# Kernel optimization log

Hardware: AMD Instinct MI355X
Metric: run time of the kernel (lower is better)

## Reference

```python
import jax, jax.numpy as jnp
import numpy as np

VOCAB = 50257
FEAT = 512
EPS = 1e-12  # F.normalize default eps


def setup_inputs() -> dict:
    key = jax.random.key(0)
    k1, k2, k3 = jax.random.split(key, 3)
    token_ids = jax.random.randint(k1, (32, 4096), 0, VOCAB)
    # nn.Linear(vocab, feat): weight [FEAT, VOCAB], bias [FEAT]
    W = jax.random.normal(k2, (FEAT, VOCAB), dtype=jnp.float32) * 0.02
    b = jax.random.normal(k3, (FEAT,), dtype=jnp.float32) * 0.02
    return {"token_ids": token_ids, "W": W, "b": b}


def reference(token_ids, W, b):
    # one_hot(ids) @ W.T + b  ==  gather rows of W.T at ids, then add bias
    feats = W.T[token_ids] + b  # [B, S, FEAT]
    norm = jnp.sqrt(jnp.sum(feats * feats, axis=-1, keepdims=True))
    return feats / jnp.maximum(norm, EPS)
```

## Files before the change

### kernel.cpp

```cpp
#include <hip/hip_runtime.h>
#include <hip/hip_bf16.h>

#define VOCAB 50257
#define FEAT 512
#define NTOK (32 * 4096)
#define EPS 1e-12f
#define NFT 8

typedef float f32x4 __attribute__((ext_vector_type(4)));

__device__ __forceinline__ unsigned short f2bf(float x) {
    __hip_bfloat16 h = __float2bfloat16(x);
    unsigned short u; __builtin_memcpy(&u, &h, 2); return u;
}
__device__ __forceinline__ float bfround(float x) {
    return __bfloat162float(__float2bfloat16(x));
}
__device__ __forceinline__ float bflo(unsigned int w) {
    unsigned int u = w << 16; float f; __builtin_memcpy(&f, &u, 4); return f;
}
__device__ __forceinline__ float bfhi(unsigned int w) {
    unsigned int u = w & 0xffff0000u; float f; __builtin_memcpy(&f, &u, 4); return f;
}

__global__ __launch_bounds__(256) void transpose_bias_bf16(
        const float* __restrict__ W, const float* __restrict__ b,
        unsigned short* __restrict__ Wt, float* __restrict__ partial) {
    __shared__ float tile[64][65];
    __shared__ float psum[4][64];
    const int t = threadIdx.x, l = t & 63, w = t >> 6;
    const int v0 = blockIdx.x * 64, f0 = blockIdx.y * 64;
    const int c = l & 15, r = l >> 4;
    const int vb = v0 + c * 4;

    float p[4] = {0.f, 0.f, 0.f, 0.f};
#pragma unroll
    for (int k = 0; k < 4; ++k) {
        const int fl = w * 16 + k * 4 + r;
        const int f  = f0 + fl;
        f32x4 x;
        if (vb + 3 < VOCAB) {
            __builtin_memcpy(&x, W + (size_t)f * VOCAB + vb, 16);
        } else {
#pragma unroll
            for (int q = 0; q < 4; ++q)
                x[q] = (vb + q < VOCAB) ? W[(size_t)f * VOCAB + vb + q] : 0.0f;
        }
        const float bf = b[f];
#pragma unroll
        for (int q = 0; q < 4; ++q) {
            const float xi = x[q] + bf;
            tile[fl][c * 4 + q] = xi;
            const float xr = bfround(xi);
            p[q] += xr * xr;
        }
    }
#pragma unroll
    for (int q = 0; q < 4; ++q) {
        float s = p[q];
        s += __shfl_xor(s, 16, 64);
        s += __shfl_xor(s, 32, 64);
        if (r == 0) psum[w][c * 4 + q] = s;
    }
    __syncthreads();
    if (t < 64) {
        const int v = v0 + t;
        if (v < VOCAB)
            partial[blockIdx.y * VOCAB + v] =
                psum[0][t] + psum[1][t] + psum[2][t] + psum[3][t];
    }
#pragma unroll
    for (int ps = 0; ps < 2; ++ps) {
        const int idx = t + 256 * ps;
        const int vl = idx >> 3, ch = idx & 7;
        const int v = v0 + vl;
        if (v < VOCAB) {
            unsigned int pk[4];
#pragma unroll
            for (int j = 0; j < 4; ++j) {
                const int f = ch * 8 + 2 * j;
                pk[j] = (unsigned int)f2bf(tile[f][vl]) |
                        ((unsigned int)f2bf(tile[f + 1][vl]) << 16);
            }
            *(uint4*)(Wt + (size_t)v * FEAT + f0 + ch * 8) =
                make_uint4(pk[0], pk[1], pk[2], pk[3]);
        }
    }
}

__global__ __launch_bounds__(256) void norm_table(const float* __restrict__ partial,
                                                  float* __restrict__ invn) {
    const int v = blockIdx.x * 256 + threadIdx.x;
    if (v >= VOCAB) return;
    float s = 0.0f;
#pragma unroll
    for (int j = 0; j < NFT; ++j) s += partial[j * VOCAB + v];
    invn[v] = 1.0f / fmaxf(sqrtf(s), EPS);
}

__global__ __launch_bounds__(256) void encode_bf16_ilp2(
        const int* __restrict__ ids, const unsigned short* __restrict__ Wt,
        const float* __restrict__ invn, float* __restrict__ out) {
    const int wv   = (int)((blockIdx.x * (unsigned long long)blockDim.x + threadIdx.x) >> 6);
    const int lane = threadIdx.x & 63;
    const int tok0 = wv * 2;
    if (tok0 >= NTOK) return;

    const int id0 = ids[tok0];
    const int id1 = ids[tok0 + 1];

    const uint4 r0 = *((const uint4*)(Wt + (size_t)id0 * FEAT) + lane);
    const uint4 r1 = *((const uint4*)(Wt + (size_t)id1 * FEAT) + lane);
    const float i0 = invn[id0];
    const float i1 = invn[id1];

    f32x4 a0 = {bflo(r0.x) * i0, bfhi(r0.x) * i0, bflo(r0.y) * i0, bfhi(r0.y) * i0};
    f32x4 a1 = {bflo(r0.z) * i0, bfhi(r0.z) * i0, bflo(r0.w) * i0, bfhi(r0.w) * i0};
    f32x4 c0 = {bflo(r1.x) * i1, bfhi(r1.x) * i1, bflo(r1.y) * i1, bfhi(r1.y) * i1};
    f32x4 c1 = {bflo(r1.z) * i1, bfhi(r1.z) * i1, bflo(r1.w) * i1, bfhi(r1.w) * i1};

    f32x4* d0 = (f32x4*)(out + (size_t)tok0 * FEAT + lane * 8);
    f32x4* d1 = (f32x4*)(out + (size_t)(tok0 + 1) * FEAT + lane * 8);
    d0[0] = a0;
    d0[1] = a1;
    d1[0] = c0;
    d1[1] = c1;
}

__global__ __launch_bounds__(256) void encode_direct(const int* __restrict__ ids,
                                                     const float* __restrict__ W,
                                                     const float* __restrict__ bias,
                                                     float* __restrict__ out) {
    const int tok  = (int)((blockIdx.x * (unsigned long long)blockDim.x + threadIdx.x) >> 6);
    const int lane = threadIdx.x & 63;
    if (tok >= NTOK) return;
    const int id = ids[tok];
    float x[8];
    float s = 0.0f;
#pragma unroll
    for (int j = 0; j < 8; ++j) {
        const int f = lane * 8 + j;
        x[j] = W[(size_t)f * VOCAB + id] + bias[f];
        s += x[j] * x[j];
    }
#pragma unroll
    for (int off = 32; off > 0; off >>= 1)
        s += __shfl_xor(s, off, 64);
    const float inv = 1.0f / fmaxf(sqrtf(s), EPS);
    float4 o0 = make_float4(x[0] * inv, x[1] * inv, x[2] * inv, x[3] * inv);
    float4 o1 = make_float4(x[4] * inv, x[5] * inv, x[6] * inv, x[7] * inv);
    float4* dst = (float4*)(out + (size_t)tok * FEAT + lane * 8);
    dst[0] = o0;
    dst[1] = o1;
}

extern "C" void kernel_launch(void* const* d_in, const int* in_sizes, int n_in,
                              void* d_out, int out_size, void* d_ws, size_t ws_size,
                              hipStream_t stream) {
    const int*   ids  = (const int*)d_in[0];
    const float* W    = (const float*)d_in[1];
    const float* bias = (const float*)d_in[2];
    float*       out  = (float*)d_out;

    const size_t wt_bytes   = (size_t)VOCAB * FEAT * sizeof(unsigned short);
    const size_t part_bytes = (size_t)NFT * VOCAB * sizeof(float);
    const size_t inv_bytes  = (size_t)VOCAB * sizeof(float);

    if (ws_size >= wt_bytes + part_bytes + inv_bytes) {
        unsigned short* Wt = (unsigned short*)d_ws;
        float* partial     = (float*)((char*)d_ws + wt_bytes);
        float* invn        = (float*)((char*)d_ws + wt_bytes + part_bytes);
        dim3 tgrid((VOCAB + 63) / 64, FEAT / 64);
        transpose_bias_bf16<<<tgrid, 256, 0, stream>>>(W, bias, Wt, partial);
        norm_table<<<(VOCAB + 255) / 256, 256, 0, stream>>>(partial, invn);
        encode_bf16_ilp2<<<NTOK / 8, 256, 0, stream>>>(ids, Wt, invn, out);
    } else {
        encode_direct<<<NTOK / 4, 256, 0, stream>>>(ids, W, bias, out);
    }
}
```

Before: 109.3 us.

## Fuse norm table into transpose kernel and raise encode ILP to four tokens

The transpose kernel now loops over all eight feature tiles within one block per vocab slice, accumulating the squared-norm sum in registers and writing the inverse norm directly. This removes the separate norm_table launch and the partial-sum buffer round trip. The encode kernel now handles four tokens per wavefront instead of two, putting more loads in flight. The trade-off is a transpose grid eight times smaller (about 786 blocks), which may reduce parallelism and latency hiding in the transpose phase.

```diff
diff --git a/kernel.cpp b/kernel.cpp
--- a/kernel.cpp
+++ b/kernel.cpp
@@ -23,38 +23,63 @@
     unsigned int u = w & 0xffff0000u; float f; __builtin_memcpy(&f, &u, 4); return f;
 }
 
-__global__ __launch_bounds__(256) void transpose_bias_bf16(
+__global__ __launch_bounds__(256) void transpose_bias_norm_bf16(
         const float* __restrict__ W, const float* __restrict__ b,
-        unsigned short* __restrict__ Wt, float* __restrict__ partial) {
+        unsigned short* __restrict__ Wt, float* __restrict__ invn) {
     __shared__ float tile[64][65];
     __shared__ float psum[4][64];
     const int t = threadIdx.x, l = t & 63, w = t >> 6;
-    const int v0 = blockIdx.x * 64, f0 = blockIdx.y * 64;
+    const int v0 = blockIdx.x * 64;
     const int c = l & 15, r = l >> 4;
     const int vb = v0 + c * 4;
 
     float p[4] = {0.f, 0.f, 0.f, 0.f};
+
+    for (int ft = 0; ft < NFT; ++ft) {
+        const int f0 = ft * 64;
+        __syncthreads();
 #pragma unroll
-    for (int k = 0; k < 4; ++k) {
-        const int fl = w * 16 + k * 4 + r;
-        const int f  = f0 + fl;
-        f32x4 x;
-        if (vb + 3 < VOCAB) {
-            __builtin_memcpy(&x, W + (size_t)f * VOCAB + vb, 16);
-        } else {
+        for (int k = 0; k < 4; ++k) {
+            const int fl = w * 16 + k * 4 + r;
+            const int f  = f0 + fl;
+            f32x4 x;
+            if (vb + 3 < VOCAB) {
+                __builtin_memcpy(&x, W + (size_t)f * VOCAB + vb, 16);
+            } else {
 #pragma unroll
-            for (int q = 0; q < 4; ++q)
-                x[q] = (vb + q < VOCAB) ? W[(size_t)f * VOCAB + vb + q] : 0.0f;
+                for (int q = 0; q < 4; ++q)
+                    x[q] = (vb + q < VOCAB) ? W[(size_t)f * VOCAB + vb + q] : 0.0f;
+            }
+            const float bf = b[f];
+#pragma unroll
+            for (int q = 0; q < 4; ++q) {
+                const float xi = x[q] + bf;
+                tile[fl][c * 4 + q] = xi;
+                const float xr = bfround(xi);
+                p[q] += xr * xr;
+            }
         }
-        const float bf = b[f];
+        __syncthreads();
+
 #pragma unroll
-        for (int q = 0; q < 4; ++q) {
-            const float xi = x[q] + bf;
-            tile[fl][c * 4 + q] = xi;
-            const float xr = bfround(xi);
-            p[q] += xr * xr;
+        for (int ps = 0; ps < 2; ++ps) {
+            const int idx = t + 256 * ps;
+            const int vl = idx >> 3, ch = idx & 7;
+            const int v = v0 + vl;
+            if (v < VOCAB) {
+                unsigned int pk[4];
+#pragma unroll
+                for (int j = 0; j < 4; ++j) {
+                    const int f = ch * 8 + 2 * j;
+                    pk[j] = (unsigned int)f2bf(tile[f][vl]) |
+                            ((unsigned int)f2bf(tile[f + 1][vl]) << 16);
+                }
+                *(uint4*)(Wt + (size_t)v * FEAT + f0 + ch * 8) =
+                    make_uint4(pk[0], pk[1], pk[2], pk[3]);
+            }
         }
     }
+
 #pragma unroll
     for (int q = 0; q < 4; ++q) {
         float s = p[q];
@@ -65,66 +90,44 @@
     __syncthreads();
     if (t < 64) {
         const int v = v0 + t;
-        if (v < VOCAB)
-            partial[blockIdx.y * VOCAB + v] =
-                psum[0][t] + psum[1][t] + psum[2][t] + psum[3][t];
-    }
-#pragma unroll
-    for (int ps = 0; ps < 2; ++ps) {
-        const int idx = t + 256 * ps;
-        const int vl = idx >> 3, ch = idx & 7;
-        const int v = v0 + vl;
         if (v < VOCAB) {
-            unsigned int pk[4];
-#pragma unroll
-            for (int j = 0; j < 4; ++j) {
-                const int f = ch * 8 + 2 * j;
-                pk[j] = (unsigned int)f2bf(tile[f][vl]) |
-                        ((unsigned int)f2bf(tile[f + 1][vl]) << 16);
-            }
-            *(uint4*)(Wt + (size_t)v * FEAT + f0 + ch * 8) =
-                make_uint4(pk[0], pk[1], pk[2], pk[3]);
+            const float s = psum[0][t] + psum[1][t] + psum[2][t] + psum[3][t];
+            invn[v] = 1.0f / fmaxf(sqrtf(s), EPS);
         }
     }
 }
 
-__global__ __launch_bounds__(256) void norm_table(const float* __restrict__ partial,
-                                                  float* __restrict__ invn) {
-    const int v = blockIdx.x * 256 + threadIdx.x;
-    if (v >= VOCAB) return;
-    float s = 0.0f;
-#pragma unroll
-    for (int j = 0; j < NFT; ++j) s += partial[j * VOCAB + v];
-    invn[v] = 1.0f / fmaxf(sqrtf(s), EPS);
-}
-
-__global__ __launch_bounds__(256) void encode_bf16_ilp2(
+__global__ __launch_bounds__(256) void encode_bf16_ilp4(
         const int* __restrict__ ids, const unsigned short* __restrict__ Wt,
         const float* __restrict__ invn, float* __restrict__ out) {
     const int wv   = (int)((blockIdx.x * (unsigned long long)blockDim.x + threadIdx.x) >> 6);
     const int lane = threadIdx.x & 63;
-    const int tok0 = wv * 2;
+    const int tok0 = wv * 4;
     if (tok0 >= NTOK) return;
 
-    const int id0 = ids[tok0];
-    const int id1 = ids[tok0 + 1];
+    int id[4];
+#pragma unroll
+    for (int i = 0; i < 4; ++i) id[i] = ids[tok0 + i];
 
-    const uint4 r0 = *((const uint4*)(Wt + (size_t)id0 * FEAT) + lane);
-    const uint4 r1 = *((const uint4*)(Wt + (size_t)id1 * FEAT) + lane);
-    const float i0 = invn[id0];
-    const float i1 = invn[id1];
+    uint4 rr[4];
+#pragma unroll
+    for (int i = 0; i < 4; ++i)
+        rr[i] = *((const uint4*)(Wt + (size_t)id[i] * FEAT) + lane);
 
-    f32x4 a0 = {bflo(r0.x) * i0, bfhi(r0.x) * i0, bflo(r0.y) * i0, bfhi(r0.y) * i0};
-    f32x4 a1 = {bflo(r0.z) * i0, bfhi(r0.z) * i0, bflo(r0.w) * i0, bfhi(r0.w) * i0};
-    f32x4 c0 = {bflo(r1.x) * i1, bfhi(r1.x) * i1, bflo(r1.y) * i1, bfhi(r1.y) * i1};
-    f32x4 c1 = {bflo(r1.z) * i1, bfhi(r1.z) * i1, bflo(r1.w) * i1, bfhi(r1.w) * i1};
+    float iv[4];
+#pragma unroll
+    for (int i = 0; i < 4; ++i) iv[i] = invn[id[i]];
 
-    f32x4* d0 = (f32x4*)(out + (size_t)tok0 * FEAT + lane * 8);
-    f32x4* d1 = (f32x4*)(out + (size_t)(tok0 + 1) * FEAT + lane * 8);
-    d0[0] = a0;
-    d0[1] = a1;
-    d1[0] = c0;
-    d1[1] = c1;
+#pragma unroll
+    for (int i = 0; i < 4; ++i) {
+        f32x4 o0 = {bflo(rr[i].x) * iv[i], bfhi(rr[i].x) * iv[i],
+                    bflo(rr[i].y) * iv[i], bfhi(rr[i].y) * iv[i]};
+        f32x4 o1 = {bflo(rr[i].z) * iv[i], bfhi(rr[i].z) * iv[i],
+                    bflo(rr[i].w) * iv[i], bfhi(rr[i].w) * iv[i]};
+        f32x4* dst = (f32x4*)(out + (size_t)(tok0 + i) * FEAT + lane * 8);
+        dst[0] = o0;
+        dst[1] = o1;
+    }
 }
 
 __global__ __launch_bounds__(256) void encode_direct(const int* __restrict__ ids,
@@ -162,18 +165,14 @@
     const float* bias = (const float*)d_in[2];
     float*       out  = (float*)d_out;
 
-    const size_t wt_bytes   = (size_t)VOCAB * FEAT * sizeof(unsigned short);
-    const size_t part_bytes = (size_t)NFT * VOCAB * sizeof(float);
-    const size_t inv_bytes  = (size_t)VOCAB * sizeof(float);
+    const size_t wt_bytes  = (size_t)VOCAB * FEAT * sizeof(unsigned short);
+    const size_t inv_bytes = (size_t)VOCAB * sizeof(float);
 
-    if (ws_size >= wt_bytes + part_bytes + inv_bytes) {
+    if (ws_size >= wt_bytes + inv_bytes) {
         unsigned short* Wt = (unsigned short*)d_ws;
-        float* partial     = (float*)((char*)d_ws + wt_bytes);
-        float* invn        = (float*)((char*)d_ws + wt_bytes + part_bytes);
-        dim3 tgrid((VOCAB + 63) / 64, FEAT / 64);
-        transpose_bias_bf16<<<tgrid, 256, 0, stream>>>(W, bias, Wt, partial);
-        norm_table<<<(VOCAB + 255) / 256, 256, 0, stream>>>(partial, invn);
-        encode_bf16_ilp2<<<NTOK / 8, 256, 0, stream>>>(ids, Wt, invn, out);
+        float* invn        = (float*)((char*)d_ws + wt_bytes);
+        transpose_bias_norm_bf16<<<(VOCAB + 63) / 64, 256, 0, stream>>>(W, bias, Wt, invn);
+        encode_bf16_ilp4<<<NTOK / 16, 256, 0, stream>>>(ids, Wt, invn, out);
     } else {
         encode_direct<<<NTOK / 4, 256, 0, stream>>>(ids, W, bias, out);
     }
```

New measurement: 114.5 us. 1.05x slower.
